# Kernel optimization log

Measured on AMD Instinct MI355X. Metric: run time of the kernel, lower is better.

## Reference

```python
import jax, jax.numpy as jnp
import numpy as np

H = 32; W = 32; C = 128; K = 3
FS = K * K                      # filter_size = 9
CH = H - K + 1; CW = W - K + 1
F = CH * CW                     # num_convs = 900
HW = H * W                      # 1024
TEMP = 1.0                      # softmax_temp
EPS = 1e-5                      # masked_softmax epsilon
B = 8


def _build_masks():
    # local_indices[f] = flat indices of the K x K window f (row-major),
    # matching compute_input_mask with stride=1, no stochastic stride.
    idx = np.zeros((F, FS), dtype=np.int32)
    f = 0
    for i in range(CH):
        for j in range(CW):
            rows = np.arange(i, i + K)[:, None]
            cols = np.arange(j, j + K)[None, :]
            idx[f] = (rows * W + cols).reshape(-1)
            f += 1
    # global mask = (1 - local_mask) * (1 - padding_mask); padding_mask == 0 for 'valid'
    gmask = np.ones((F, HW), dtype=np.float32)
    gmask[np.arange(F)[:, None], idx] = 0.0
    return jnp.asarray(idx), jnp.asarray(gmask)


def setup_inputs() -> dict:
    key = jax.random.key(0)
    ks = jax.random.split(key, 8)
    bound = 1.0 / np.sqrt(C)  # torch nn.Linear default init
    u = lambda k, shape: jax.random.uniform(k, shape, jnp.float32, -bound, bound)
    batch = jax.random.normal(ks[0], (B, H, W, C), jnp.float32)
    Wq = u(ks[1], (C, C)); bq = u(ks[2], (C,))
    Wk = u(ks[3], (C, C)); bk = u(ks[4], (C,))
    wv = u(ks[5], (C, 1)); bv = u(ks[6], (1,))
    local_indices, gmask = _build_masks()
    return {"batch": batch, "Wq": Wq, "bq": bq, "Wk": Wk, "bk": bk,
            "wv": wv, "bv": bv, "gmask": gmask, "local_indices": local_indices}


def reference(batch, Wq, bq, Wk, bk, wv, bv, gmask, local_indices):
    # Approach '4': per-window local queries attend over global (non-window)
    # pixels; scalar values gate the local patch pixels; gated patch sums to
    # one output pixel per window. Valid padding => local pixels are unmasked
    # and the masked softmax zeroes out window/padding positions, so the
    # per-window masked linear transforms reduce exactly to full-image
    # transforms gathered/masked afterwards (no [F,B,H,W,C] materialization).
    b = batch.shape[0]
    xf = batch.reshape(b, HW, C)
    Q = xf @ Wq.T + bq                         # [B,HW,C] query_transform
    Kf = xf @ Wk.T + bk                        # [B,HW,C] key_transform
    V = (xf @ wv + bv)[..., 0]                 # [B,HW]   value_transform (C->1)
    Qg = Q[:, local_indices]                   # [B,F,FS,C] local queries (gather)
    Xl = xf[:, local_indices]                  # [B,F,FS,C] local patch features
    compat = jnp.einsum('bfpc,bqc->bfpq', Qg, Kf) / TEMP   # [B,F,FS,HW]
    # masked_softmax: exp * mask / (sum + eps), no max-subtraction (faithful)
    exps = jnp.exp(compat) * gmask[None, :, None, :]
    attn = exps / (exps.sum(-1, keepdims=True) + EPS)
    gates = jnp.einsum('bfpq,bq->bfp', attn, V)            # [B,F,FS] scalar gates
    out = jnp.einsum('bfp,bfpc->bfc', gates, Xl)           # [B,F,C]
    return out.reshape(b, CH, CW, C)
```

## Files before the change

### kernel.cpp

```cpp
#include <hip/hip_runtime.h>

#define BATCH 8
#define HW_N  1024
#define CD    128
#define W_IMG 32
#define CH_O  30
#define F_N   900

#define OFF_QH 0u
#define OFF_QL 2097152u
#define OFF_KH 4194304u
#define OFF_KL 6291456u
#define OFF_V  8388608u
#define OFF_D  8421376u
#define OFF_T  9240576u
#define OFF_TV 9306112u

typedef __bf16 bf16x8 __attribute__((ext_vector_type(8)));
typedef float  f32x4  __attribute__((ext_vector_type(4)));

__global__ __launch_bounds__(256) void qkv_kernel(
    const float* __restrict__ xf,
    const float* __restrict__ Wq, const float* __restrict__ bq,
    const float* __restrict__ Wk, const float* __restrict__ bk,
    const float* __restrict__ wv, const float* __restrict__ bv,
    __bf16* __restrict__ Qh, __bf16* __restrict__ Ql,
    __bf16* __restrict__ Kh, __bf16* __restrict__ Kl,
    float* __restrict__ V)
{
    __shared__ float xs[32][132];
    __shared__ float wqs[32][132];
    __shared__ float wks[32][132];
    const int t = threadIdx.x;
    const int rowbase = blockIdx.x * 32;

#pragma unroll
    for (int m = 0; m < 4; ++m) {
        int id = t + 256 * m;
        int r  = id >> 5;
        int kq = id & 31;
        *(float4*)&xs[r][kq * 4] =
            *(const float4*)&xf[(size_t)(rowbase + r) * CD + kq * 4];
    }

    const int tx = t & 15, ty = t >> 4;

    for (int cc = 0; cc < 4; ++cc) {
        __syncthreads();
#pragma unroll
        for (int m = 0; m < 4; ++m) {
            int id = t + 256 * m;
            int r  = id >> 5;
            int kq = id & 31;
            *(float4*)&wqs[r][kq * 4] =
                *(const float4*)&Wq[(size_t)(cc * 32 + r) * CD + kq * 4];
            *(float4*)&wks[r][kq * 4] =
                *(const float4*)&Wk[(size_t)(cc * 32 + r) * CD + kq * 4];
        }
        __syncthreads();

        float aq[2][2], ak[2][2];
#pragma unroll
        for (int j = 0; j < 2; ++j)
#pragma unroll
            for (int m = 0; m < 2; ++m) { aq[j][m] = 0.f; ak[j][m] = 0.f; }

#pragma unroll 8
        for (int k = 0; k < CD; k += 4) {
            float4 x[2], q[2], kk[2];
            x[0]  = *(const float4*)&xs[ty][k];
            x[1]  = *(const float4*)&xs[ty + 16][k];
            q[0]  = *(const float4*)&wqs[tx][k];
            q[1]  = *(const float4*)&wqs[tx + 16][k];
            kk[0] = *(const float4*)&wks[tx][k];
            kk[1] = *(const float4*)&wks[tx + 16][k];
#pragma unroll
            for (int j = 0; j < 2; ++j)
#pragma unroll
                for (int m = 0; m < 2; ++m) {
                    aq[j][m] += x[j].x * q[m].x + x[j].y * q[m].y +
                                x[j].z * q[m].z + x[j].w * q[m].w;
                    ak[j][m] += x[j].x * kk[m].x + x[j].y * kk[m].y +
                                x[j].z * kk[m].z + x[j].w * kk[m].w;
                }
        }

#pragma unroll
        for (int j = 0; j < 2; ++j)
#pragma unroll
            for (int m = 0; m < 2; ++m) {
                int r = ty + 16 * j;
                int c = cc * 32 + tx + 16 * m;
                size_t o = (size_t)(rowbase + r) * CD + c;
                float qv = aq[j][m] + bq[c];
                float kv = ak[j][m] + bk[c];
                __bf16 qh = (__bf16)qv; float qhf = (float)qh;
                __bf16 ql = (__bf16)(qv - qhf);
                __bf16 khv = (__bf16)kv; float khf = (float)khv;
                __bf16 klv = (__bf16)(kv - khf);
                Qh[o] = qh;  Ql[o] = ql;
                Kh[o] = khv; Kl[o] = klv;
            }
    }

    __syncthreads();
    if (t < 32) {
        float s = 0.f;
#pragma unroll 8
        for (int k = 0; k < CD; ++k) s += xs[t][k] * wv[k];
        V[rowbase + t] = s + bv[0];
    }
}

#define A_LDS_H 0
#define A_LDS_L 18432
#define B_LDS_H 36864
#define B_LDS_L 55296
#define VS_LDS  73728
#define ATTN_LDS_TOTAL 74240
#define SCR_TV_OFF 16896

__global__ __launch_bounds__(256, 2) void attn_kernel(
    const __bf16* __restrict__ Qh, const __bf16* __restrict__ Ql,
    const __bf16* __restrict__ Kh, const __bf16* __restrict__ Kl,
    const float* __restrict__ V,
    double* __restrict__ T, double* __restrict__ TV,
    float* __restrict__ D)
{
    extern __shared__ char lds[];
    __bf16* Ah = (__bf16*)(lds + A_LDS_H);
    __bf16* Al = (__bf16*)(lds + A_LDS_L);
    __bf16* Bh = (__bf16*)(lds + B_LDS_H);
    __bf16* Bl = (__bf16*)(lds + B_LDS_L);
    float*  Vs = (float*)(lds + VS_LDS);

    const int b  = blockIdx.x;
    const int rb = blockIdx.y;
    const int cb = blockIdx.z;
    const int t  = threadIdx.x;
    const int w    = t >> 6;
    const int lane = t & 63;
    const int q    = lane >> 4;
    const int i    = lane & 15;
    const int wy = w >> 1, wx = w & 1;

    if (t < 128) Vs[t] = V[b * HW_N + cb * 128 + t];

    f32x4 acc[4][4];
#pragma unroll
    for (int r = 0; r < 4; ++r)
#pragma unroll
        for (int f = 0; f < 4; ++f) acc[r][f] = (f32x4){0.f, 0.f, 0.f, 0.f};

    const size_t abase = (size_t)(b * HW_N + rb * 128) * CD;
    const size_t bbase = (size_t)(b * HW_N + cb * 128) * CD;

    for (int khalf = 0; khalf < 2; ++khalf) {
        __syncthreads();
#pragma unroll
        for (int m = 0; m < 4; ++m) {
            int id  = t + 256 * m;
            int row = id >> 3;
            int c8  = id & 7;
            size_t gsrc = (size_t)row * CD + khalf * 64 + c8 * 8;
            int ldst = row * 72 + c8 * 8;
            *(f32x4*)&Ah[ldst] = *(const f32x4*)&Qh[abase + gsrc];
            *(f32x4*)&Al[ldst] = *(const f32x4*)&Ql[abase + gsrc];
            *(f32x4*)&Bh[ldst] = *(const f32x4*)&Kh[bbase + gsrc];
            *(f32x4*)&Bl[ldst] = *(const f32x4*)&Kl[bbase + gsrc];
        }
        __syncthreads();

#pragma unroll
        for (int kk = 0; kk < 2; ++kk) {
            bf16x8 ah[4], alr[4], bh4[4], bl4[4];
#pragma unroll
            for (int r = 0; r < 4; ++r) {
                int aoff = (wy * 64 + r * 16 + i) * 72 + kk * 32 + q * 8;
                ah[r]  = *(bf16x8*)&Ah[aoff];
                alr[r] = *(bf16x8*)&Al[aoff];
                int boff = (wx * 64 + r * 16 + i) * 72 + kk * 32 + q * 8;
                bh4[r] = *(bf16x8*)&Bh[boff];
                bl4[r] = *(bf16x8*)&Bl[boff];
            }
#pragma unroll
            for (int r = 0; r < 4; ++r)
#pragma unroll
                for (int f = 0; f < 4; ++f) {
                    acc[r][f] = __builtin_amdgcn_mfma_f32_16x16x32_bf16(
                        ah[r], bh4[f], acc[r][f], 0, 0, 0);
                    acc[r][f] = __builtin_amdgcn_mfma_f32_16x16x32_bf16(
                        ah[r], bl4[f], acc[r][f], 0, 0, 0);
                    acc[r][f] = __builtin_amdgcn_mfma_f32_16x16x32_bf16(
                        alr[r], bh4[f], acc[r][f], 0, 0, 0);
                }
        }
    }

    float st[4][4], stv[4][4];
#pragma unroll
    for (int r = 0; r < 4; ++r)
#pragma unroll
        for (int g = 0; g < 4; ++g) { st[r][g] = 0.f; stv[r][g] = 0.f; }

    const bool band = (cb - rb <= 1) && (rb - cb <= 1);

#pragma unroll
    for (int f = 0; f < 4; ++f) {
        int col_local = wx * 64 + f * 16 + i;
        int hw_c = cb * 128 + col_local;
        float v = Vs[col_local];
        int cimg_r = hw_c >> 5, cimg_c = hw_c & 31;
#pragma unroll
        for (int r = 0; r < 4; ++r)
#pragma unroll
            for (int g = 0; g < 4; ++g) {
                float e = __expf(acc[r][f][g]);
                st[r][g]  += e;
                stv[r][g] += e * v;
                if (band) {
                    int row_local = wy * 64 + r * 16 + q * 4 + g;
                    int hw_r = rb * 128 + row_local;
                    int dy = cimg_r - (hw_r >> 5);
                    int dx = cimg_c - (hw_r & 31);
                    if ((unsigned)(dy + 2) <= 4u && (unsigned)(dx + 2) <= 4u)
                        D[(size_t)(b * HW_N + hw_r) * 25 + (dy + 2) * 5 + (dx + 2)] = e;
                }
            }
    }

    __syncthreads();
    float* scrT  = (float*)lds;
    float* scrTV = (float*)(lds + SCR_TV_OFF);
#pragma unroll
    for (int r = 0; r < 4; ++r)
#pragma unroll
        for (int g = 0; g < 4; ++g) {
            int row_local = wy * 64 + r * 16 + q * 4 + g;
            scrT [row_local * 33 + wx * 16 + i] = st[r][g];
            scrTV[row_local * 33 + wx * 16 + i] = stv[r][g];
        }
    __syncthreads();
    if (t < 128) {
        double s = 0.0;
#pragma unroll
        for (int c = 0; c < 32; ++c) s += (double)scrT[t * 33 + c];
        atomicAdd(&T[b * HW_N + rb * 128 + t], s);
    } else {
        int tt = t - 128;
        double s = 0.0;
#pragma unroll
        for (int c = 0; c < 32; ++c) s += (double)scrTV[tt * 33 + c];
        atomicAdd(&TV[b * HW_N + rb * 128 + tt], s);
    }
}

__global__ __launch_bounds__(256) void gate_out_kernel(
    const float* __restrict__ xf, const float* __restrict__ V,
    const double* __restrict__ T, const double* __restrict__ TV,
    const float* __restrict__ D, float* __restrict__ out)
{
    const int fi = blockIdx.x;
    const int b  = blockIdx.y;
    const int t  = threadIdx.x;

    __shared__ float xs[96 * 128];
    __shared__ float gates[30][9];

#pragma unroll
    for (int m = 0; m < 12; ++m) {
        int id   = t + 256 * m;
        int srow = id >> 5;
        int c4   = id & 31;
        int r3   = srow >> 5, colc = srow & 31;
        *(float4*)&xs[srow * 128 + c4 * 4] =
            *(const float4*)&xf[((size_t)(b * 32 + fi + r3) * 32 + colc) * CD + c4 * 4];
    }

    for (int g = t; g < 270; g += 256) {
        int fj = g / 9, p = g % 9;
        int pr = p / 3, pc = p % 3;
        int ip = (fi + pr) * W_IMG + (fj + pc);
        const float* Drow = &D[(size_t)(b * HW_N + ip) * 25];
        double se = 0.0, sev = 0.0;
#pragma unroll
        for (int qq = 0; qq < 9; ++qq) {
            int qr = qq / 3, qc = qq % 3;
            float e = Drow[(qr - pr + 2) * 5 + (qc - pc + 2)];
            se  += (double)e;
            sev += (double)(e * V[b * HW_N + (fi + qr) * W_IMG + (fj + qc)]);
        }
        double denom = T[b * HW_N + ip] - se + 1e-5;
        double numer = TV[b * HW_N + ip] - sev;
        gates[fj][p] = (float)(numer / denom);
    }
    __syncthreads();

    const int c   = t & 127;
    const int fjg = t >> 7;
#pragma unroll
    for (int it = 0; it < 15; ++it) {
        int fj = fjg * 15 + it;
        float o = 0.f;
#pragma unroll
        for (int p = 0; p < 9; ++p) {
            int pr = p / 3, pc = p % 3;
            o += gates[fj][p] * xs[(pr * 32 + fj + pc) * 128 + c];
        }
        out[((size_t)(b * F_N) + fi * CH_O + fj) * CD + c] = o;
    }
}

extern "C" void kernel_launch(void* const* d_in, const int* in_sizes, int n_in,
                              void* d_out, int out_size, void* d_ws, size_t ws_size,
                              hipStream_t stream)
{
    (void)in_sizes; (void)n_in; (void)out_size; (void)ws_size;
    const float* batch = (const float*)d_in[0];
    const float* Wq    = (const float*)d_in[1];
    const float* bq    = (const float*)d_in[2];
    const float* Wk    = (const float*)d_in[3];
    const float* bk    = (const float*)d_in[4];
    const float* wv    = (const float*)d_in[5];
    const float* bv    = (const float*)d_in[6];

    char*    ws = (char*)d_ws;
    __bf16*  Qh = (__bf16*)(ws + OFF_QH);
    __bf16*  Ql = (__bf16*)(ws + OFF_QL);
    __bf16*  Kh = (__bf16*)(ws + OFF_KH);
    __bf16*  Kl = (__bf16*)(ws + OFF_KL);
    float*   V  = (float*)(ws + OFF_V);
    float*   D  = (float*)(ws + OFF_D);
    double*  T  = (double*)(ws + OFF_T);
    double*  TV = (double*)(ws + OFF_TV);
    float*   out = (float*)d_out;

    hipMemsetAsync(T, 0, 2 * BATCH * HW_N * sizeof(double), stream);

    qkv_kernel<<<dim3(256), dim3(256), 0, stream>>>(batch, Wq, bq, Wk, bk, wv, bv,
                                                    Qh, Ql, Kh, Kl, V);
    attn_kernel<<<dim3(8, 8, 8), dim3(256), ATTN_LDS_TOTAL, stream>>>(
        Qh, Ql, Kh, Kl, V, T, TV, D);
    gate_out_kernel<<<dim3(CH_O, BATCH), dim3(256), 0, stream>>>(batch, V, T, TV, D, out);
}
```

Before: 118.7 us.

## Store Q/K in MFMA fragment layout, load via async LDS, replace atomics with partials

The QKV kernel now writes the hi/lo bf16 Q and K in a fragment-tiled layout, so the attention kernel can stream tiles straight into LDS with global_load_lds and read MFMA operands without padded indexing. The double atomicAdd row-sum reductions become per-column-block partial writes, which the gate kernel sums, and this removes the memset. The intent is to cut global-to-register-to-LDS copy overhead, atomic contention and one launch. In exchange the gate kernel does extra partial-sum reads, and the scattered 2-byte stores in the QKV kernel may coalesce worse.

```diff
diff --git a/kernel.cpp b/kernel.cpp
--- a/kernel.cpp
+++ b/kernel.cpp
@@ -7,17 +7,29 @@
 #define CH_O  30
 #define F_N   900
 
-#define OFF_QH 0u
-#define OFF_QL 2097152u
-#define OFF_KH 4194304u
-#define OFF_KL 6291456u
-#define OFF_V  8388608u
-#define OFF_D  8421376u
-#define OFF_T  9240576u
-#define OFF_TV 9306112u
+#define OFF_QH  0u
+#define OFF_QL  2097152u
+#define OFF_KH  4194304u
+#define OFF_KL  6291456u
+#define OFF_V   8388608u
+#define OFF_D   8421376u
+#define OFF_TP  9240576u
+#define OFF_TVP 9764864u
 
 typedef __bf16 bf16x8 __attribute__((ext_vector_type(8)));
 typedef float  f32x4  __attribute__((ext_vector_type(4)));
+
+__device__ __forceinline__ size_t frag_off(int R, int c) {
+    return (size_t)(R >> 4) * 2048 +
+           (size_t)((((c >> 5) * 4 + ((c >> 3) & 3)) * 128) + ((R & 15) * 8) + (c & 7));
+}
+
+__device__ __forceinline__ void async16(const __bf16* g, __bf16* l) {
+    __builtin_amdgcn_global_load_lds(
+        (const __attribute__((address_space(1))) unsigned int*)g,
+        (__attribute__((address_space(3))) unsigned int*)l,
+        16, 0, 0);
+}
 
 __global__ __launch_bounds__(256) void qkv_kernel(
     const float* __restrict__ xf,
@@ -91,15 +103,16 @@
             for (int m = 0; m < 2; ++m) {
                 int r = ty + 16 * j;
                 int c = cc * 32 + tx + 16 * m;
-                size_t o = (size_t)(rowbase + r) * CD + c;
+                int R = rowbase + r;
+                size_t o = frag_off(R, c);
                 float qv = aq[j][m] + bq[c];
                 float kv = ak[j][m] + bk[c];
-                __bf16 qh = (__bf16)qv; float qhf = (float)qh;
-                __bf16 ql = (__bf16)(qv - qhf);
-                __bf16 khv = (__bf16)kv; float khf = (float)khv;
-                __bf16 klv = (__bf16)(kv - khf);
+                __bf16 qh = (__bf16)qv;
+                __bf16 ql = (__bf16)(qv - (float)qh);
+                __bf16 kh2 = (__bf16)kv;
+                __bf16 kl2 = (__bf16)(kv - (float)kh2);
                 Qh[o] = qh;  Ql[o] = ql;
-                Kh[o] = khv; Kl[o] = klv;
+                Kh[o] = kh2; Kl[o] = kl2;
             }
     }
 
@@ -112,27 +125,27 @@
     }
 }
 
-#define A_LDS_H 0
-#define A_LDS_L 18432
-#define B_LDS_H 36864
-#define B_LDS_L 55296
-#define VS_LDS  73728
-#define ATTN_LDS_TOTAL 74240
-#define SCR_TV_OFF 16896
+#define A_H 0
+#define A_L 16384
+#define B_H 32768
+#define B_L 49152
+#define VS_OFF 65536
+#define ATTN_LDS_TOTAL 66048
+#define SCR2 16896
 
 __global__ __launch_bounds__(256, 2) void attn_kernel(
     const __bf16* __restrict__ Qh, const __bf16* __restrict__ Ql,
     const __bf16* __restrict__ Kh, const __bf16* __restrict__ Kl,
     const float* __restrict__ V,
-    double* __restrict__ T, double* __restrict__ TV,
+    double* __restrict__ Tp, double* __restrict__ TVp,
     float* __restrict__ D)
 {
     extern __shared__ char lds[];
-    __bf16* Ah = (__bf16*)(lds + A_LDS_H);
-    __bf16* Al = (__bf16*)(lds + A_LDS_L);
-    __bf16* Bh = (__bf16*)(lds + B_LDS_H);
-    __bf16* Bl = (__bf16*)(lds + B_LDS_L);
-    float*  Vs = (float*)(lds + VS_LDS);
+    __bf16* Ah = (__bf16*)(lds + A_H);
+    __bf16* Al = (__bf16*)(lds + A_L);
+    __bf16* Bh = (__bf16*)(lds + B_H);
+    __bf16* Bl = (__bf16*)(lds + B_L);
+    float*  Vs = (float*)(lds + VS_OFF);
 
     const int b  = blockIdx.x;
     const int rb = blockIdx.y;
@@ -152,36 +165,35 @@
 #pragma unroll
         for (int f = 0; f < 4; ++f) acc[r][f] = (f32x4){0.f, 0.f, 0.f, 0.f};
 
-    const size_t abase = (size_t)(b * HW_N + rb * 128) * CD;
-    const size_t bbase = (size_t)(b * HW_N + cb * 128) * CD;
-
-    for (int khalf = 0; khalf < 2; ++khalf) {
+    const size_t abase = (size_t)(b * 8 + rb) * 16384;
+    const size_t bbase = (size_t)(b * 8 + cb) * 16384;
+
+    for (int kh = 0; kh < 2; ++kh) {
         __syncthreads();
 #pragma unroll
         for (int m = 0; m < 4; ++m) {
-            int id  = t + 256 * m;
-            int row = id >> 3;
-            int c8  = id & 7;
-            size_t gsrc = (size_t)row * CD + khalf * 64 + c8 * 8;
-            int ldst = row * 72 + c8 * 8;
-            *(f32x4*)&Ah[ldst] = *(const f32x4*)&Qh[abase + gsrc];
-            *(f32x4*)&Al[ldst] = *(const f32x4*)&Ql[abase + gsrc];
-            *(f32x4*)&Bh[ldst] = *(const f32x4*)&Kh[bbase + gsrc];
-            *(f32x4*)&Bl[ldst] = *(const f32x4*)&Kl[bbase + gsrc];
-        }
+            int id = t + 256 * m;
+            size_t goff = (size_t)(id >> 7) * 2048 + kh * 1024 + (id & 127) * 8;
+            int loff = id * 8;
+            async16(Qh + abase + goff, Ah + loff);
+            async16(Ql + abase + goff, Al + loff);
+            async16(Kh + bbase + goff, Bh + loff);
+            async16(Kl + bbase + goff, Bl + loff);
+        }
+        asm volatile("s_waitcnt vmcnt(0)" ::: "memory");
         __syncthreads();
 
 #pragma unroll
-        for (int kk = 0; kk < 2; ++kk) {
-            bf16x8 ah[4], alr[4], bh4[4], bl4[4];
+        for (int kcl = 0; kcl < 2; ++kcl) {
+            bf16x8 ah[4], al4[4], bh4[4], bl4[4];
 #pragma unroll
             for (int r = 0; r < 4; ++r) {
-                int aoff = (wy * 64 + r * 16 + i) * 72 + kk * 32 + q * 8;
-                ah[r]  = *(bf16x8*)&Ah[aoff];
-                alr[r] = *(bf16x8*)&Al[aoff];
-                int boff = (wx * 64 + r * 16 + i) * 72 + kk * 32 + q * 8;
-                bh4[r] = *(bf16x8*)&Bh[boff];
-                bl4[r] = *(bf16x8*)&Bl[boff];
+                int ao = (((wy * 4 + r) * 2 + kcl) * 4 + q) * 128 + i * 8;
+                ah[r]  = *(bf16x8*)&Ah[ao];
+                al4[r] = *(bf16x8*)&Al[ao];
+                int bo = (((wx * 4 + r) * 2 + kcl) * 4 + q) * 128 + i * 8;
+                bh4[r] = *(bf16x8*)&Bh[bo];
+                bl4[r] = *(bf16x8*)&Bl[bo];
             }
 #pragma unroll
             for (int r = 0; r < 4; ++r)
@@ -192,7 +204,7 @@
                     acc[r][f] = __builtin_amdgcn_mfma_f32_16x16x32_bf16(
                         ah[r], bl4[f], acc[r][f], 0, 0, 0);
                     acc[r][f] = __builtin_amdgcn_mfma_f32_16x16x32_bf16(
-                        alr[r], bh4[f], acc[r][f], 0, 0, 0);
+                        al4[r], bh4[f], acc[r][f], 0, 0, 0);
                 }
         }
     }
@@ -231,41 +243,42 @@
 
     __syncthreads();
     float* scrT  = (float*)lds;
-    float* scrTV = (float*)(lds + SCR_TV_OFF);
+    float* scrTV = (float*)(lds + SCR2);
 #pragma unroll
     for (int r = 0; r < 4; ++r)
 #pragma unroll
         for (int g = 0; g < 4; ++g) {
-            int row_local = wy * 64 + r * 16 + q * 4 + g;
-            scrT [row_local * 33 + wx * 16 + i] = st[r][g];
-            scrTV[row_local * 33 + wx * 16 + i] = stv[r][g];
+            int rl = wy * 64 + r * 16 + q * 4 + g;
+            scrT [rl * 33 + wx * 16 + i] = st[r][g];
+            scrTV[rl * 33 + wx * 16 + i] = stv[r][g];
         }
     __syncthreads();
     if (t < 128) {
         double s = 0.0;
 #pragma unroll
         for (int c = 0; c < 32; ++c) s += (double)scrT[t * 33 + c];
-        atomicAdd(&T[b * HW_N + rb * 128 + t], s);
+        Tp[(size_t)(b * HW_N + rb * 128 + t) * 8 + cb] = s;
     } else {
         int tt = t - 128;
         double s = 0.0;
 #pragma unroll
         for (int c = 0; c < 32; ++c) s += (double)scrTV[tt * 33 + c];
-        atomicAdd(&TV[b * HW_N + rb * 128 + tt], s);
+        TVp[(size_t)(b * HW_N + rb * 128 + tt) * 8 + cb] = s;
     }
 }
 
 __global__ __launch_bounds__(256) void gate_out_kernel(
     const float* __restrict__ xf, const float* __restrict__ V,
-    const double* __restrict__ T, const double* __restrict__ TV,
+    const double* __restrict__ Tp, const double* __restrict__ TVp,
     const float* __restrict__ D, float* __restrict__ out)
 {
     const int fi = blockIdx.x;
     const int b  = blockIdx.y;
     const int t  = threadIdx.x;
 
-    __shared__ float xs[96 * 128];
-    __shared__ float gates[30][9];
+    __shared__ float  xs[96 * 128];
+    __shared__ float  gates[30][9];
+    __shared__ double Ts[96], TVs[96];
 
 #pragma unroll
     for (int m = 0; m < 12; ++m) {
@@ -277,9 +290,26 @@
             *(const float4*)&xf[((size_t)(b * 32 + fi + r3) * 32 + colc) * CD + c4 * 4];
     }
 
+    if (t < 96) {
+        int R = b * HW_N + (fi + (t >> 5)) * W_IMG + (t & 31);
+        double s = 0.0;
+#pragma unroll
+        for (int c = 0; c < 8; ++c) s += Tp[(size_t)R * 8 + c];
+        Ts[t] = s;
+    } else if (t >= 128 && t < 224) {
+        int tt = t - 128;
+        int R = b * HW_N + (fi + (tt >> 5)) * W_IMG + (tt & 31);
+        double s = 0.0;
+#pragma unroll
+        for (int c = 0; c < 8; ++c) s += TVp[(size_t)R * 8 + c];
+        TVs[tt] = s;
+    }
+    __syncthreads();
+
     for (int g = t; g < 270; g += 256) {
         int fj = g / 9, p = g % 9;
         int pr = p / 3, pc = p % 3;
+        int lrow = pr * 32 + fj + pc;
         int ip = (fi + pr) * W_IMG + (fj + pc);
         const float* Drow = &D[(size_t)(b * HW_N + ip) * 25];
         double se = 0.0, sev = 0.0;
@@ -290,8 +320,8 @@
             se  += (double)e;
             sev += (double)(e * V[b * HW_N + (fi + qr) * W_IMG + (fj + qc)]);
         }
-        double denom = T[b * HW_N + ip] - se + 1e-5;
-        double numer = TV[b * HW_N + ip] - sev;
+        double denom = Ts[lrow] - se + 1e-5;
+        double numer = TVs[lrow] - sev;
         gates[fj][p] = (float)(numer / denom);
     }
     __syncthreads();
@@ -324,22 +354,20 @@
     const float* wv    = (const float*)d_in[5];
     const float* bv    = (const float*)d_in[6];
 
-    char*    ws = (char*)d_ws;
-    __bf16*  Qh = (__bf16*)(ws + OFF_QH);
-    __bf16*  Ql = (__bf16*)(ws + OFF_QL);
-    __bf16*  Kh = (__bf16*)(ws + OFF_KH);
-    __bf16*  Kl = (__bf16*)(ws + OFF_KL);
-    float*   V  = (float*)(ws + OFF_V);
-    float*   D  = (float*)(ws + OFF_D);
-    double*  T  = (double*)(ws + OFF_T);
-    double*  TV = (double*)(ws + OFF_TV);
+    char*    ws  = (char*)d_ws;
+    __bf16*  Qh  = (__bf16*)(ws + OFF_QH);
+    __bf16*  Ql  = (__bf16*)(ws + OFF_QL);
+    __bf16*  Kh  = (__bf16*)(ws + OFF_KH);
+    __bf16*  Kl  = (__bf16*)(ws + OFF_KL);
+    float*   V   = (float*)(ws + OFF_V);
+    float*   D   = (float*)(ws + OFF_D);
+    double*  Tp  = (double*)(ws + OFF_TP);
+    double*  TVp = (double*)(ws + OFF_TVP);
     float*   out = (float*)d_out;
-
-    hipMemsetAsync(T, 0, 2 * BATCH * HW_N * sizeof(double), stream);
 
     qkv_kernel<<<dim3(256), dim3(256), 0, stream>>>(batch, Wq, bq, Wk, bk, wv, bv,
                                                     Qh, Ql, Kh, Kl, V);
     attn_kernel<<<dim3(8, 8, 8), dim3(256), ATTN_LDS_TOTAL, stream>>>(
-        Qh, Ql, Kh, Kl, V, T, TV, D);
-    gate_out_kernel<<<dim3(CH_O, BATCH), dim3(256), 0, stream>>>(batch, V, T, TV, D, out);
-}
+        Qh, Ql, Kh, Kl, V, Tp, TVp, D);
+    gate_out_kernel<<<dim3(CH_O, BATCH), dim3(256), 0, stream>>>(batch, V, Tp, TVp, D, out);
+}
```

Result: no change. 119.1 us (+0.3%).
